# Kernel optimization log

Hardware: AMD Instinct MI355X
Metric: run time of the kernel (lower is better)

## Reference

```python
import jax, jax.numpy as jnp
import numpy as np

DIM = 1024
HEADS = 16
MLP = 4096
EPS = 1e-5

def _layer_norm(x, g, b):
    mu = jnp.mean(x, axis=-1, keepdims=True)
    var = jnp.mean(jnp.square(x - mu), axis=-1, keepdims=True)
    return (x - mu) * jax.lax.rsqrt(var + EPS) * g + b

def setup_inputs() -> dict:
    key = jax.random.key(0)
    ks = jax.random.split(key, 8)
    s = 0.02
    return {
        "x": jax.random.normal(ks[0], (2, 2048, DIM), dtype=jnp.float32),
        "ln1_g": jnp.ones((DIM,), jnp.float32),
        "ln1_b": jnp.zeros((DIM,), jnp.float32),
        "qkv_w": jax.random.normal(ks[1], (DIM, 3 * DIM), jnp.float32) * s,
        "qkv_b": jnp.zeros((3 * DIM,), jnp.float32),
        "proj_w": jax.random.normal(ks[2], (DIM, DIM), jnp.float32) * s,
        "proj_b": jnp.zeros((DIM,), jnp.float32),
        "ln2_g": jnp.ones((DIM,), jnp.float32),
        "ln2_b": jnp.zeros((DIM,), jnp.float32),
        "fc1_w": jax.random.normal(ks[3], (DIM, MLP), jnp.float32) * s,
        "fc1_b": jnp.zeros((MLP,), jnp.float32),
        "fc2_w": jax.random.normal(ks[4], (MLP, DIM), jnp.float32) * s,
        "fc2_b": jnp.zeros((DIM,), jnp.float32),
    }

def reference(x, ln1_g, ln1_b, qkv_w, qkv_b, proj_w, proj_b,
              ln2_g, ln2_b, fc1_w, fc1_b, fc2_w, fc2_b):
    B, N, C = x.shape
    H = HEADS
    D = C // H
    # --- attention (pre-norm); NOTE: source applies no 1/sqrt(D) scaling ---
    h = _layer_norm(x, ln1_g, ln1_b)
    qkv = (h @ qkv_w + qkv_b).reshape(B, N, 3, H, D)
    q, k, v = (qkv[:, :, 0], qkv[:, :, 1], qkv[:, :, 2])  # [B,N,H,D]
    qk = jnp.einsum('bnhd,bmhd->bhnm', q, k)
    attn = jax.nn.softmax(qk, axis=-1)
    y = jnp.einsum('bhnm,bmhd->bnhd', attn, v).reshape(B, N, C)
    y = y @ proj_w + proj_b
    x = x + y
    # --- MLP (pre-norm), exact GELU like torch nn.GELU ---
    h2 = _layer_norm(x, ln2_g, ln2_b)
    h2 = jax.nn.gelu(h2 @ fc1_w + fc1_b, approximate=False)
    x = x + (h2 @ fc2_w + fc2_b)
    return x
```

## Files before the change

### kernel.cpp

```cpp
#include <hip/hip_runtime.h>
#include <hip/hip_bf16.h>

#define CDIM   1024
#define NSEQ   2048
#define NHEAD  16
#define HDIM   64
#define MLPDIM 4096
#define TROWS  4096

typedef __attribute__((ext_vector_type(8)))  __bf16 bf16x8;
typedef __attribute__((ext_vector_type(4)))  float  f32x4;
typedef __attribute__((ext_vector_type(16))) float  f32x16;
typedef __attribute__((ext_vector_type(4)))  unsigned short us4;

static __device__ __forceinline__ unsigned short f2bf(float f) {
  unsigned int u = __float_as_uint(f);
  u += 0x7fffu + ((u >> 16) & 1u);
  return (unsigned short)(u >> 16);
}

#define MFMA16(a, b, c) __builtin_amdgcn_mfma_f32_16x16x32_bf16(a, b, c, 0, 0, 0)
#define MFMA32(a, b, c) __builtin_amdgcn_mfma_f32_32x32x16_bf16(a, b, c, 0, 0, 0)

static __device__ __forceinline__ void gll16(const unsigned short* g, unsigned short* l) {
  __builtin_amdgcn_global_load_lds(
      (const __attribute__((address_space(1))) unsigned int*)g,
      (__attribute__((address_space(3))) unsigned int*)l, 16, 0, 0);
}

__global__ __launch_bounds__(256)
void ln_bf16_kernel(const float* __restrict__ x,
                    const float* __restrict__ gam,
                    const float* __restrict__ bet,
                    unsigned short* __restrict__ out)
{
  int row = blockIdx.x;
  int t = threadIdx.x;
  const float4* xr = (const float4*)(x + (size_t)row * CDIM);
  float4 v = xr[t];
  float s  = v.x + v.y + v.z + v.w;
  float s2 = v.x*v.x + v.y*v.y + v.z*v.z + v.w*v.w;
  #pragma unroll
  for (int off = 32; off > 0; off >>= 1) {
    s  += __shfl_down(s, off);
    s2 += __shfl_down(s2, off);
  }
  __shared__ float rs[4], rs2[4];
  int wave = t >> 6, lane = t & 63;
  if (lane == 0) { rs[wave] = s; rs2[wave] = s2; }
  __syncthreads();
  float fs  = rs[0] + rs[1] + rs[2] + rs[3];
  float fs2 = rs2[0] + rs2[1] + rs2[2] + rs2[3];
  float mu   = fs * (1.0f / CDIM);
  float var  = fs2 * (1.0f / CDIM) - mu * mu;
  float rstd = rsqrtf(var + 1e-5f);
  float4 gg = ((const float4*)gam)[t];
  float4 bb = ((const float4*)bet)[t];
  us4 o;
  o.x = f2bf((v.x - mu) * rstd * gg.x + bb.x);
  o.y = f2bf((v.y - mu) * rstd * gg.y + bb.y);
  o.z = f2bf((v.z - mu) * rstd * gg.z + bb.z);
  o.w = f2bf((v.w - mu) * rstd * gg.w + bb.w);
  ((us4*)(out + (size_t)row * CDIM))[t] = o;
}

__global__ __launch_bounds__(256)
void ln_add_bf16_kernel(float* __restrict__ x, const float* __restrict__ pp,
                        const float* __restrict__ gam, const float* __restrict__ bet,
                        unsigned short* __restrict__ out)
{
  int row = blockIdx.x;
  int t = threadIdx.x;
  float4* xr = (float4*)(x + (size_t)row * CDIM);
  const float4* pr = (const float4*)(pp + (size_t)row * CDIM);
  float4 v = xr[t];
  float4 q = pr[t];
  v.x += q.x; v.y += q.y; v.z += q.z; v.w += q.w;
  xr[t] = v;
  float s  = v.x + v.y + v.z + v.w;
  float s2 = v.x*v.x + v.y*v.y + v.z*v.z + v.w*v.w;
  #pragma unroll
  for (int off = 32; off > 0; off >>= 1) {
    s  += __shfl_down(s, off);
    s2 += __shfl_down(s2, off);
  }
  __shared__ float rs[4], rs2[4];
  int wave = t >> 6, lane = t & 63;
  if (lane == 0) { rs[wave] = s; rs2[wave] = s2; }
  __syncthreads();
  float fs  = rs[0] + rs[1] + rs[2] + rs[3];
  float fs2 = rs2[0] + rs2[1] + rs2[2] + rs2[3];
  float mu   = fs * (1.0f / CDIM);
  float var  = fs2 * (1.0f / CDIM) - mu * mu;
  float rstd = rsqrtf(var + 1e-5f);
  float4 gg = ((const float4*)gam)[t];
  float4 bb = ((const float4*)bet)[t];
  us4 o;
  o.x = f2bf((v.x - mu) * rstd * gg.x + bb.x);
  o.y = f2bf((v.y - mu) * rstd * gg.y + bb.y);
  o.z = f2bf((v.z - mu) * rstd * gg.z + bb.z);
  o.w = f2bf((v.w - mu) * rstd * gg.w + bb.w);
  ((us4*)(out + (size_t)row * CDIM))[t] = o;
}

__global__ __launch_bounds__(256)
void wt_all_kernel(const float* __restrict__ W0, unsigned short* __restrict__ T0,
                   const float* __restrict__ W1, unsigned short* __restrict__ T1,
                   const float* __restrict__ W2, unsigned short* __restrict__ T2,
                   const float* __restrict__ W3, unsigned short* __restrict__ T3)
{
  int id = blockIdx.x;
  const float* W; unsigned short* Wt; int K, N, nx;
  if (id < 3072)      { W = W0; Wt = T0; K = 1024; N = 3072; nx = 96; }
  else if (id < 4096) { W = W1; Wt = T1; K = 1024; N = 1024; nx = 32; id -= 3072; }
  else if (id < 8192) { W = W2; Wt = T2; K = 1024; N = 4096; nx = 128; id -= 4096; }
  else                { W = W3; Wt = T3; K = 4096; N = 1024; nx = 32; id -= 8192; }
  int n0 = (id % nx) * 32, k0 = (id / nx) * 32;

  __shared__ float tile[32][33];
  int t = threadIdx.x;
  int r = t >> 3, c4 = (t & 7) << 2;
  float4 v = *(const float4*)(W + (size_t)(k0 + r) * N + n0 + c4);
  tile[r][c4 + 0] = v.x; tile[r][c4 + 1] = v.y;
  tile[r][c4 + 2] = v.z; tile[r][c4 + 3] = v.w;
  __syncthreads();
  us4 o;
  o.x = f2bf(tile[c4 + 0][r]);
  o.y = f2bf(tile[c4 + 1][r]);
  o.z = f2bf(tile[c4 + 2][r]);
  o.w = f2bf(tile[c4 + 3][r]);
  *(us4*)(Wt + (size_t)(n0 + r) * K + k0 + c4) = o;
}

template<int EPI>
__global__ __launch_bounds__(256, 4)
void gemm_bt(const unsigned short* __restrict__ A, const unsigned short* __restrict__ Bt,
             const float* __restrict__ bias, int Kstride, int Kc, int nbx, int nby,
             float* __restrict__ outf, unsigned short* __restrict__ outb,
             const float* __restrict__ resid, float* __restrict__ pp,
             unsigned short* __restrict__ qo, unsigned short* __restrict__ ko,
             unsigned short* __restrict__ vo)
{
  __shared__ unsigned short As[2][128 * 32];
  __shared__ unsigned short Bs[2][128 * 32];
  const int tid  = threadIdx.x;
  const int lane = tid & 63;
  const int wave = tid >> 6;
  const int wr = wave >> 1, wc = wave & 1;
  const int g = lane >> 4, r16 = lane & 15;

  const int nwg = gridDim.x;
  const int orig = ((int)blockIdx.x & 7) * (nwg >> 3) + ((int)blockIdx.x >> 3);
  const int bx = orig % nbx;
  const int t2 = orig / nbx;
  const int by = t2 % nby;
  const int kz = t2 / nby;
  const int bm = by * 128, bn = bx * 128;
  const int kbase = kz * Kc;
  const int N = nbx * 128;

  auto stage = [&](int d, int k0) {
    #pragma unroll
    for (int c = 0; c < 2; c++) {
      int o   = (c * 256 + tid) << 3;
      int row = o >> 5;
      int col = o & 31;
      int ub  = (c * 256 + (tid & ~63)) << 3;
      gll16(A  + (size_t)(bm + row) * Kstride + kbase + k0 + col, &As[d][ub]);
      gll16(Bt + (size_t)(bn + row) * Kstride + kbase + k0 + col, &Bs[d][ub]);
    }
  };

  f32x4 acc[4][4];
  #pragma unroll
  for (int i = 0; i < 4; i++)
    #pragma unroll
    for (int j = 0; j < 4; j++) acc[i][j] = (f32x4){0.f, 0.f, 0.f, 0.f};

  stage(0, 0);
  const int nkt = Kc / 32;
  for (int kt = 0; kt < nkt; kt++) {
    const int cur = kt & 1;
    __syncthreads();
    if (kt + 1 < nkt) stage(cur ^ 1, (kt + 1) * 32);
    bf16x8 af[4], bfr[4];
    #pragma unroll
    for (int i = 0; i < 4; i++) {
      int row = wr * 64 + i * 16 + r16;
      af[i] = *(const bf16x8*)(&As[cur][row * 32 + 8 * g]);
    }
    #pragma unroll
    for (int j = 0; j < 4; j++) {
      int row = wc * 64 + j * 16 + r16;
      bfr[j] = *(const bf16x8*)(&Bs[cur][row * 32 + 8 * g]);
    }
    __builtin_amdgcn_s_setprio(1);
    #pragma unroll
    for (int i = 0; i < 4; i++)
      #pragma unroll
      for (int j = 0; j < 4; j++)
        acc[i][j] = MFMA16(af[i], bfr[j], acc[i][j]);
    __builtin_amdgcn_s_setprio(0);
  }

  if (EPI == 1 && bn >= 2048) {
    unsigned short* T = (unsigned short*)&As[0][0];
    __syncthreads();
    #pragma unroll
    for (int i = 0; i < 4; i++) {
      #pragma unroll
      for (int j = 0; j < 4; j++) {
        int col_l = wc * 64 + j * 16 + r16;
        float bv = bias[bn + col_l];
        #pragma unroll
        for (int jj = 0; jj < 4; jj++) {
          int row = wr * 64 + i * 16 + 4 * g + jj;
          *(unsigned short*)((char*)T + col_l * 256 + ((row * 2) ^ ((col_l & 7) << 4))) =
              f2bf(acc[i][j][jj] + bv);
        }
      }
    }
    __syncthreads();
    int bb = bm >> 11, tk0 = bm & 2047;
    #pragma unroll
    for (int c = 0; c < 32; c++) {
      int col_l = wave * 32 + c;
      int cv = (bn - 2048) + col_l;
      int hh = cv >> 6, d = cv & 63;
      unsigned v2 = *(unsigned*)((char*)T + col_l * 256 + ((lane * 4) ^ ((col_l & 7) << 4)));
      *(unsigned*)(vo + ((size_t)(bb * NHEAD + hh) * HDIM + d) * NSEQ + tk0 + lane * 2) = v2;
    }
    return;
  }

  #pragma unroll
  for (int i = 0; i < 4; i++) {
    #pragma unroll
    for (int j = 0; j < 4; j++) {
      int col = bn + wc * 64 + j * 16 + r16;
      float bv = (EPI == 2 && kz != 0) ? 0.f : bias[col];
      #pragma unroll
      for (int jj = 0; jj < 4; jj++) {
        int row = bm + wr * 64 + i * 16 + 4 * g + jj;
        float val = acc[i][j][jj] + bv;
        if (EPI == 1) {
          int cc = col & 1023;
          int hh = cc >> 6, d = cc & 63;
          int b = row >> 11, tk = row & 2047;
          size_t hb = (size_t)(b * NHEAD + hh);
          if (col < 1024) qo[(hb * NSEQ + tk) * HDIM + d] = f2bf(val * 1.4426950408889634f);
          else            ko[(hb * NSEQ + tk) * HDIM + d] = f2bf(val);
        } else if (EPI == 2) {
          size_t idx = (size_t)row * N + col;
          if (kz == 0) outf[idx] = val + resid[idx];
          else         pp[idx]   = val;
        } else {
          float vv = val * val;
          float u2 = val * (2.3022361f + 0.1029445f * vv);
          float ge = val - val / (1.0f + exp2f(u2));
          outb[(size_t)row * N + col] = f2bf(ge);
        }
      }
    }
  }
}

__global__ __launch_bounds__(256)
void add_kernel(float* __restrict__ out, const float* __restrict__ pp, int n4)
{
  int i = blockIdx.x * 256 + threadIdx.x;
  int stride = gridDim.x * 256;
  for (; i < n4; i += stride) {
    float4 a = ((const float4*)out)[i];
    float4 b = ((const float4*)pp)[i];
    a.x += b.x; a.y += b.y; a.z += b.z; a.w += b.w;
    ((float4*)out)[i] = a;
  }
}

__global__ __launch_bounds__(256, 4)
void attn_kernel(const unsigned short* __restrict__ q, const unsigned short* __restrict__ k,
                 const unsigned short* __restrict__ vt, unsigned short* __restrict__ y)
{
  int bid = blockIdx.x;
  int xcd = bid & 7, loc = bid >> 3;
  int bh  = xcd * 4 + (loc >> 5);
  int qb64 = loc & 31;
  int b = bh >> 4, h = bh & 15;
  int wave = threadIdx.x >> 6, lane = threadIdx.x & 63;
  int qt = wave >> 1, kvh = wave & 1;
  int ql = lane & 31;
  int hi = lane >> 5;
  int q0 = qb64 * 64 + qt * 32;
  const int kvbase = kvh * (NSEQ / 2);
  const unsigned short* qb = q  + (size_t)bh * NSEQ * HDIM;
  const unsigned short* kb = k  + (size_t)bh * NSEQ * HDIM;
  const unsigned short* vb = vt + (size_t)bh * HDIM * NSEQ;

  __shared__ unsigned short KL[2][2][2048];
  __shared__ unsigned short VL[2][2][2048];

  auto stage = [&](int d, int it) {
    int kv0 = kvbase + it * 32;
    #pragma unroll
    for (int i = 0; i < 2; i++) {
      int c = i * 128 + qt * 64 + lane;
      int row = c >> 3, col = c & 7;
      int sc  = (row << 3) | (col ^ (row & 7));
      gll16(kb + (size_t)kv0 * HDIM + sc * 8, &KL[kvh][d][(i * 128 + qt * 64) * 8]);
    }
    #pragma unroll
    for (int i = 0; i < 2; i++) {
      int c = i * 128 + qt * 64 + lane;
      int row = c >> 2, col = c & 3;
      int scol = col ^ ((row >> 1) & 3);
      gll16(vb + (size_t)row * NSEQ + kv0 + scol * 8, &VL[kvh][d][(i * 128 + qt * 64) * 8]);
    }
  };

  bf16x8 aq[4];
  #pragma unroll
  for (int s = 0; s < 4; s++)
    aq[s] = *(const bf16x8*)(qb + (size_t)(q0 + ql) * HDIM + s * 16 + hi * 8);

  float ssum = 0.f;
  f32x16 o0, o1;
  #pragma unroll
  for (int r = 0; r < 16; r++) { o0[r] = 0.f; o1[r] = 0.f; }

  stage(0, 0);
  const int nit = NSEQ / 64;
  for (int it = 0; it < nit; it++) {
    const int cur = it & 1;
    __syncthreads();
    if (it + 1 < nit) stage(cur ^ 1, it + 1);
    bf16x8 kf[4];
    #pragma unroll
    for (int s = 0; s < 4; s++)
      kf[s] = *(const bf16x8*)((const char*)KL[kvh][cur] +
               ql * 128 + ((((s << 1) | hi) ^ (ql & 7)) << 4));
    f32x16 sacc;
    #pragma unroll
    for (int r = 0; r < 16; r++) sacc[r] = -32.0f;
    __builtin_amdgcn_s_setprio(1);
    #pragma unroll
    for (int s = 0; s < 4; s++)
      sacc = MFMA32(kf[s], aq[s], sacc);
    __builtin_amdgcn_s_setprio(0);
    float ps = 0.f;
    #pragma unroll
    for (int r = 0; r < 16; r++) {
      sacc[r] = exp2f(sacc[r]);
      ps += sacc[r];
    }
    ssum += ps;
    bf16x8 vf[2][2];
    #pragma unroll
    for (int t = 0; t < 2; t++)
      #pragma unroll
      for (int db = 0; db < 2; db++)
        vf[t][db] = *(const bf16x8*)((const char*)VL[kvh][cur] +
                     (db * 32 + ql) * 64 + ((((t << 1) | hi) ^ ((ql >> 1) & 3)) << 4));
    __builtin_amdgcn_s_setprio(1);
    #pragma unroll
    for (int t = 0; t < 2; t++) {
      unsigned pk01, pk23, pk45, pk67;
      asm("v_cvt_pk_bf16_f32 %0, %1, %2" : "=v"(pk01) : "v"(sacc[8*t+0]), "v"(sacc[8*t+1]));
      asm("v_cvt_pk_bf16_f32 %0, %1, %2" : "=v"(pk23) : "v"(sacc[8*t+2]), "v"(sacc[8*t+3]));
      asm("v_cvt_pk_bf16_f32 %0, %1, %2" : "=v"(pk45) : "v"(sacc[8*t+4]), "v"(sacc[8*t+5]));
      asm("v_cvt_pk_bf16_f32 %0, %1, %2" : "=v"(pk67) : "v"(sacc[8*t+6]), "v"(sacc[8*t+7]));
      asm("v_permlane32_swap_b32 %0, %1" : "+v"(pk01), "+v"(pk45));
      asm("v_permlane32_swap_b32 %0, %1" : "+v"(pk23), "+v"(pk67));
      union { unsigned u[4]; bf16x8 v; } pf;
      pf.u[0] = pk01; pf.u[1] = pk23; pf.u[2] = pk45; pf.u[3] = pk67;
      o0 = MFMA32(vf[t][0], pf.v, o0);
      o1 = MFMA32(vf[t][1], pf.v, o1);
    }
    __builtin_amdgcn_s_setprio(0);
  }

  __syncthreads();
  float* OM = (float*)&KL[0][0][0];
  float* SM = (float*)&VL[0][0][0];
  if (kvh == 1) {
    #pragma unroll
    for (int r = 0; r < 16; r++) {
      OM[r * 128 + qt * 64 + lane]        = o0[r];
      OM[(16 + r) * 128 + qt * 64 + lane] = o1[r];
    }
    SM[qt * 64 + lane] = ssum;
  }
  __syncthreads();
  if (kvh == 0) {
    float st = ssum + SM[qt * 64 + lane];
    st += __shfl_xor(st, 32);
    float inv = 1.0f / st;
    #pragma unroll
    for (int r = 0; r < 16; r++) {
      o0[r] += OM[r * 128 + qt * 64 + lane];
      o1[r] += OM[(16 + r) * 128 + qt * 64 + lane];
    }
    unsigned short* yr = y + ((size_t)(b * NSEQ + q0 + ql)) * CDIM + h * HDIM;
    #pragma unroll
    for (int db = 0; db < 2; db++) {
      const f32x16& oo = db ? o1 : o0;
      #pragma unroll
      for (int rq = 0; rq < 4; rq++) {
        us4 w;
        w.x = f2bf(oo[4*rq+0] * inv);
        w.y = f2bf(oo[4*rq+1] * inv);
        w.z = f2bf(oo[4*rq+2] * inv);
        w.w = f2bf(oo[4*rq+3] * inv);
        *(us4*)(yr + db * 32 + rq * 8 + hi * 4) = w;
      }
    }
  }
}

extern "C" void kernel_launch(void* const* d_in, const int* in_sizes, int n_in,
                              void* d_out, int out_size, void* d_ws, size_t ws_size,
                              hipStream_t stream)
{
  const float* x      = (const float*)d_in[0];
  const float* ln1_g  = (const float*)d_in[1];
  const float* ln1_b  = (const float*)d_in[2];
  const float* qkv_w  = (const float*)d_in[3];
  const float* qkv_b  = (const float*)d_in[4];
  const float* proj_w = (const float*)d_in[5];
  const float* proj_b = (const float*)d_in[6];
  const float* ln2_g  = (const float*)d_in[7];
  const float* ln2_b  = (const float*)d_in[8];
  const float* fc1_w  = (const float*)d_in[9];
  const float* fc1_b  = (const float*)d_in[10];
  const float* fc2_w  = (const float*)d_in[11];
  const float* fc2_b  = (const float*)d_in[12];
  float* out = (float*)d_out;

  char* p = (char*)d_ws;
  size_t off = 0;
  auto alloc = [&](size_t bytes) -> void* {
    void* r = p + off; off += (bytes + 255) & ~(size_t)255; return r;
  };
  unsigned short* wt_qkv  = (unsigned short*)alloc((size_t)3072 * 1024 * 2);
  unsigned short* wt_proj = (unsigned short*)alloc((size_t)1024 * 1024 * 2);
  unsigned short* wt_fc1  = (unsigned short*)alloc((size_t)4096 * 1024 * 2);
  unsigned short* wt_fc2  = (unsigned short*)alloc((size_t)1024 * 4096 * 2);
  unsigned short* h1  = (unsigned short*)alloc((size_t)TROWS * CDIM * 2);
  unsigned short* qb  = (unsigned short*)alloc((size_t)TROWS * CDIM * 2);
  unsigned short* kb  = (unsigned short*)alloc((size_t)TROWS * CDIM * 2);
  unsigned short* vtb = (unsigned short*)alloc((size_t)TROWS * CDIM * 2);
  unsigned short* yb  = (unsigned short*)alloc((size_t)TROWS * CDIM * 2);
  float*          x1  = (float*)alloc((size_t)TROWS * CDIM * 4);
  unsigned short* h2  = (unsigned short*)alloc((size_t)TROWS * CDIM * 2);
  unsigned short* g1  = (unsigned short*)alloc((size_t)TROWS * MLPDIM * 2);
  float* pp = (float*)qb;

  dim3 blk(256);
  wt_all_kernel<<<dim3(12288), blk, 0, stream>>>(
      qkv_w, wt_qkv, proj_w, wt_proj, fc1_w, wt_fc1, fc2_w, wt_fc2);
  ln_bf16_kernel<<<TROWS, blk, 0, stream>>>(x, ln1_g, ln1_b, h1);
  gemm_bt<1><<<dim3(768), blk, 0, stream>>>(
      h1, wt_qkv, qkv_b, 1024, 1024, 24, 32,
      nullptr, nullptr, nullptr, nullptr, qb, kb, vtb);
  attn_kernel<<<dim3(1024), blk, 0, stream>>>(qb, kb, vtb, yb);
  gemm_bt<2><<<dim3(512), blk, 0, stream>>>(
      yb, wt_proj, proj_b, 1024, 512, 8, 32,
      x1, nullptr, x, pp, nullptr, nullptr, nullptr);
  ln_add_bf16_kernel<<<TROWS, blk, 0, stream>>>(x1, pp, ln2_g, ln2_b, h2);
  gemm_bt<3><<<dim3(1024), blk, 0, stream>>>(
      h2, wt_fc1, fc1_b, 1024, 1024, 32, 32,
      nullptr, g1, nullptr, nullptr, nullptr, nullptr, nullptr);
  gemm_bt<2><<<dim3(512), blk, 0, stream>>>(
      g1, wt_fc2, fc2_b, 4096, 2048, 8, 32,
      out, nullptr, x1, pp, nullptr, nullptr, nullptr);
  add_kernel<<<dim3(2048), blk, 0, stream>>>(out, pp, TROWS * CDIM / 4);
}
```

Baseline: 275.7 us.

## Add dedicated 256x256-tile FC1 GEMM kernel with 512 threads and GELU epilogue

```diff
diff --git a/kernel.cpp b/kernel.cpp
--- a/kernel.cpp
+++ b/kernel.cpp
@@ -265,6 +265,95 @@
   }
 }
 
+__global__ __launch_bounds__(512, 1)
+void gemm_fc1(const unsigned short* __restrict__ A, const unsigned short* __restrict__ Bt,
+              const float* __restrict__ bias, unsigned short* __restrict__ outb)
+{
+  __shared__ unsigned short As[2][256 * 32];
+  __shared__ unsigned short Bs[2][256 * 32];
+  const int tid  = threadIdx.x;
+  const int lane = tid & 63;
+  const int wave = tid >> 6;
+  const int wr = wave >> 2, wc = wave & 3;
+  const int g = lane >> 4, r16 = lane & 15;
+  const int K = 1024, N = MLPDIM;
+
+  const int nwg = gridDim.x;
+  const int orig = ((int)blockIdx.x & 7) * (nwg >> 3) + ((int)blockIdx.x >> 3);
+  const int bx = orig & 15, by = orig >> 4;
+  const int bm = by * 256, bn = bx * 256;
+
+  auto stage = [&](int d, int kt) {
+    int k0 = kt * 32;
+    #pragma unroll
+    for (int l = 0; l < 2; l++) {
+      int p   = l * 512 + tid;
+      int row = p >> 2, cc = p & 3;
+      int scc = cc ^ (row & 3);
+      int ub  = (l * 512 + (tid & ~63)) << 3;
+      gll16(A  + (size_t)(bm + row) * K + k0 + (scc << 3), &As[d][ub]);
+      gll16(Bt + (size_t)(bn + row) * K + k0 + (scc << 3), &Bs[d][ub]);
+    }
+  };
+
+  f32x4 acc[8][4];
+  #pragma unroll
+  for (int i = 0; i < 8; i++)
+    #pragma unroll
+    for (int j = 0; j < 4; j++) acc[i][j] = (f32x4){0.f, 0.f, 0.f, 0.f};
+
+  stage(0, 0);
+  stage(1, 1);
+  const int nkt = K / 32;
+  for (int kt = 0; kt < nkt; kt++) {
+    const int cur = kt & 1;
+    if (kt + 1 < nkt) asm volatile("s_waitcnt vmcnt(4)" ::: "memory");
+    else              asm volatile("s_waitcnt vmcnt(0)" ::: "memory");
+    __builtin_amdgcn_s_barrier();
+    asm volatile("" ::: "memory");
+    bf16x8 af[8], bfr[4];
+    #pragma unroll
+    for (int i = 0; i < 8; i++) {
+      int row = wr * 128 + i * 16 + r16;
+      af[i] = *(const bf16x8*)((const char*)&As[cur][0] + row * 64 + ((g ^ (row & 3)) << 4));
+    }
+    #pragma unroll
+    for (int j = 0; j < 4; j++) {
+      int row = wc * 64 + j * 16 + r16;
+      bfr[j] = *(const bf16x8*)((const char*)&Bs[cur][0] + row * 64 + ((g ^ (row & 3)) << 4));
+    }
+    asm volatile("s_waitcnt lgkmcnt(0)" ::: "memory");
+    __builtin_amdgcn_s_barrier();
+    asm volatile("" ::: "memory");
+    if (kt + 2 < nkt) stage(cur, kt + 2);
+    __builtin_amdgcn_s_setprio(1);
+    #pragma unroll
+    for (int i = 0; i < 8; i++)
+      #pragma unroll
+      for (int j = 0; j < 4; j++)
+        acc[i][j] = MFMA16(af[i], bfr[j], acc[i][j]);
+    __builtin_amdgcn_s_setprio(0);
+  }
+
+  #pragma unroll
+  for (int i = 0; i < 8; i++) {
+    #pragma unroll
+    for (int j = 0; j < 4; j++) {
+      int col = bn + wc * 64 + j * 16 + r16;
+      float bv = bias[col];
+      #pragma unroll
+      for (int jj = 0; jj < 4; jj++) {
+        int row = bm + wr * 128 + i * 16 + 4 * g + jj;
+        float val = acc[i][j][jj] + bv;
+        float vv = val * val;
+        float u2 = val * (2.3022361f + 0.1029445f * vv);
+        float ge = val - val / (1.0f + exp2f(u2));
+        outb[(size_t)row * N + col] = f2bf(ge);
+      }
+    }
+  }
+}
+
 __global__ __launch_bounds__(256)
 void add_kernel(float* __restrict__ out, const float* __restrict__ pp, int n4)
 {
@@ -467,9 +556,7 @@
       yb, wt_proj, proj_b, 1024, 512, 8, 32,
       x1, nullptr, x, pp, nullptr, nullptr, nullptr);
   ln_add_bf16_kernel<<<TROWS, blk, 0, stream>>>(x1, pp, ln2_g, ln2_b, h2);
-  gemm_bt<3><<<dim3(1024), blk, 0, stream>>>(
-      h2, wt_fc1, fc1_b, 1024, 1024, 32, 32,
-      nullptr, g1, nullptr, nullptr, nullptr, nullptr, nullptr);
+  gemm_fc1<<<dim3(256), dim3(512), 0, stream>>>(h2, wt_fc1, fc1_b, g1);
   gemm_bt<2><<<dim3(512), blk, 0, stream>>>(
       g1, wt_fc2, fc2_b, 4096, 2048, 8, 32,
       out, nullptr, x1, pp, nullptr, nullptr, nullptr);
```

Measured after the change: 274.8 us. No clear change (-0.3%).
